# Kernel optimization log

Measured on AMD Instinct MI355X. Metric: run time of the kernel, lower is better.

Reference implementation:

```python
import jax, jax.numpy as jnp
import numpy as np

B, T, H = 128, 1024, 200
IN0, OUT = 8, 4  # GRU layer-0 input size (4 targets + 4 emotion), fc output dim


def setup_inputs() -> dict:
    key = jax.random.key(0)
    ks = jax.random.split(key, 12)
    s = 1.0 / np.sqrt(H)  # torch RNN default init: U(-1/sqrt(H), 1/sqrt(H))
    u = lambda k, shp: jax.random.uniform(k, shp, jnp.float32, -s, s)
    return {
        "x": jax.random.normal(ks[0], (B, T, IN0), jnp.float32),
        "W_ih0": u(ks[1], (3 * H, IN0)),
        "W_hh0": u(ks[2], (3 * H, H)),
        "b_ih0": u(ks[3], (3 * H,)),
        "b_hh0": u(ks[4], (3 * H,)),
        "W_ih1": u(ks[5], (3 * H, H)),
        "W_hh1": u(ks[6], (3 * H, H)),
        "b_ih1": u(ks[7], (3 * H,)),
        "b_hh1": u(ks[8], (3 * H,)),
        "W_fc": u(ks[9], (OUT, H)),
        "b_fc": u(ks[10], (OUT,)),
        "xlens": jax.random.randint(ks[11], (B,), 1, T + 1),
    }


def _gru_cell(h, gx, W_hh, b_hh):
    # torch GRU cell: gx = W_ih @ x + b_ih precomputed, gates order [r, z, n]
    gh = h @ W_hh.T + b_hh
    ir, iz, i_n = jnp.split(gx, 3, axis=-1)
    hr, hz, hn = jnp.split(gh, 3, axis=-1)
    r = jax.nn.sigmoid(ir + hr)
    z = jax.nn.sigmoid(iz + hz)
    n = jnp.tanh(i_n + r * hn)
    return (1.0 - z) * n + z * h


def _forward(x, W_ih0, W_hh0, b_ih0, b_hh0, W_ih1, W_hh1, b_ih1, b_hh1, W_fc, b_fc):
    b, t, _ = x.shape
    emotion = x[:, 0, -4:]                      # (B,4) frozen at t=0, as in source
    targets = x[:, :, :4]                       # (B,T,4)
    # step inputs: t=0 -> ones(B,4); t>0 -> targets[:, t-1] (teacher forcing)
    tf = jnp.concatenate([jnp.ones((b, 1, 4), x.dtype), targets[:, :-1, :]], axis=1)
    inputs = jnp.concatenate(
        [tf, jnp.broadcast_to(emotion[:, None, :], (b, t, 4))], axis=-1)  # (B,T,8)
    # precompute layer-0 input projections for all steps (one big GEMM)
    gx0 = jnp.einsum("btc,gc->btg", inputs, W_ih0) + b_ih0  # (B,T,3H)

    def step(carry, gx0_t):
        h0, h1 = carry
        h0 = _gru_cell(h0, gx0_t, W_hh0, b_hh0)
        gx1 = h0 @ W_ih1.T + b_ih1
        h1 = _gru_cell(h1, gx1, W_hh1, b_hh1)
        out = jnp.tanh(h1 @ W_fc.T + b_fc)      # fused fc + tanh
        return (h0, h1), out

    h0 = jnp.zeros((b, H), x.dtype)
    h1 = jnp.zeros((b, H), x.dtype)
    _, outs = jax.lax.scan(step, (h0, h1), jnp.swapaxes(gx0, 0, 1))  # (T,B,4)
    return jnp.swapaxes(outs, 0, 1)             # (B,T,4)


def reference(x, W_ih0, W_hh0, b_ih0, b_hh0, W_ih1, W_hh1, b_ih1, b_hh1, W_fc, b_fc, xlens):
    # xlens is accepted but unused, exactly as in the source forward()
    return _forward(x, W_ih0, W_hh0, b_ih0, b_hh0, W_ih1, W_hh1, b_ih1, b_hh1, W_fc, b_fc)
```

## Files before the change

kernel.cpp:

```cpp
#include <hip/hip_runtime.h>
#include <hip/hip_bf16.h>


#define TT 1024
#define HH 200
#define NB 16
#define HS 13
#define KP 232

typedef __attribute__((ext_vector_type(8))) short short8;
typedef __attribute__((ext_vector_type(4))) float f32x4;

__device__ __forceinline__ float sigm(float v) { return 1.0f / (1.0f + __expf(-v)); }
__device__ __forceinline__ float tanh_fast(float v) {
  float e = __expf(-2.0f * v);
  return (1.0f - e) / (1.0f + e);
}
__device__ __forceinline__ uint llc_load_u32(const uint* p) {
  return __hip_atomic_load(p, __ATOMIC_RELAXED, __HIP_MEMORY_SCOPE_SYSTEM);
}
__device__ __forceinline__ void llc_store_u32(uint* p, uint v) {
  __hip_atomic_store(p, v, __ATOMIC_RELAXED, __HIP_MEMORY_SCOPE_SYSTEM);
}
__device__ __forceinline__ float bfu2f(ushort u) {
  return __uint_as_float(((uint)u) << 16);
}
__device__ __forceinline__ ushort f2bfu(float f) {
  __hip_bfloat16 b = __float2bfloat16(f);
  return *(ushort*)&b;
}
__device__ __forceinline__ uint packf(float h) {
  ushort hi = f2bfu(h);
  float  fh = bfu2f(hi);
  ushort lo = f2bfu(h - fh);
  return (uint)hi | ((uint)lo << 16);
}

__global__ __launch_bounds__(256, 1) void gru2_mfma(
    const float* __restrict__ x,
    const float* __restrict__ Wih0, const float* __restrict__ Whh0,
    const float* __restrict__ bih0, const float* __restrict__ bhh0,
    const float* __restrict__ Wih1, const float* __restrict__ Whh1,
    const float* __restrict__ bih1, const float* __restrict__ bhh1,
    const float* __restrict__ Wfc,  const float* __restrict__ bfc,
    float* __restrict__ out,
    uint* __restrict__ h0g, uint* __restrict__ h1g, uint* __restrict__ syncp)
{
  __shared__ __align__(16) ushort hBh[2][NB][KP];
  __shared__ __align__(16) ushort hBl[2][NB][KP];
  __shared__ float D[117][17];
  __shared__ float Wi0t[8][39];
  __shared__ float bi0[39], bh0[39], bi1[39], bh1[39], bfs[4];
  __shared__ float xc[NB][8];

  const int tid  = threadIdx.x;
  const int wave = tid >> 6;
  const int lane = tid & 63;
  const int m15  = lane & 15;
  const int q    = lane >> 4;

  const int g  = blockIdx.x & 7;
  const int s  = blockIdx.x >> 3;
  const int b0 = g * NB;
  const int j0 = s * HS;
  const int hs = (HH - j0 < HS) ? (HH - j0) : HS;
  const int th   = 3 * hs;
  const int h0r  = 6 * hs;
  const int T0   = (h0r + 15) >> 4;
  const int NT   = T0 + ((th + 15) >> 4);
  const bool isOut = (s == 15);

  uint* flags = syncp;

  short8 Ah[2][7], Al[2][7];
  #pragma unroll
  for (int mt = 0; mt < 2; ++mt) {
    const int T = wave * 2 + mt;
    const bool fc  = isOut && (wave == 2) && (mt == 0);
    const bool val = fc || (T < NT);
    #pragma unroll
    for (int kt = 0; kt < 7; ++kt) {
      short8 vh = {0,0,0,0,0,0,0,0}, vl = {0,0,0,0,0,0,0,0};
      #pragma unroll
      for (int j = 0; j < 8; ++j) {
        const int k = kt * 32 + q * 8 + j;
        float w = 0.0f;
        if (val && k < HH) {
          if (fc) {
            if (m15 < 4) w = Wfc[m15 * HH + k];
          } else {
            const int p = T * 16 + m15;
            int r = -1;
            if (p < h0r) r = p;
            else if (p >= T0 * 16 && (p - T0 * 16) < th) r = h0r + (p - T0 * 16);
            if (r >= 0) {
              const int m  = r / th, rr = r - m * th;
              const int qq = rr / hs, jj = rr - qq * hs;
              const float* src = (m == 0) ? Whh0 : ((m == 1) ? Wih1 : Whh1);
              w = src[(qq * HH + j0 + jj) * HH + k];
            }
          }
        }
        const ushort uh = f2bfu(w);
        const ushort ul = f2bfu(w - bfu2f(uh));
        vh[j] = (short)uh; vl[j] = (short)ul;
      }
      Ah[mt][kt] = vh; Al[mt][kt] = vl;
    }
  }

  for (int u = tid; u < th * 8; u += 256) {
    int rr = u >> 3, c = u & 7;
    int qq = rr / hs, jj = rr - qq * hs;
    Wi0t[c][rr] = Wih0[(qq * HH + j0 + jj) * 8 + c];
  }
  for (int u = tid; u < th; u += 256) {
    int qq = u / hs, jj = u - qq * hs;
    int grow = qq * HH + j0 + jj;
    bi0[u] = bih0[grow]; bh0[u] = bhh0[grow];
    bi1[u] = bih1[grow]; bh1[u] = bhh1[grow];
  }
  if (tid < 4) bfs[tid] = bfc[tid];
  for (int u = tid; u < 2 * NB * KP / 2; u += 256) ((uint*)hBh)[u] = 0;
  for (int u = tid; u < 2 * NB * KP / 2; u += 256) ((uint*)hBl)[u] = 0;
  if (tid < 128 && (tid & 7) >= 4)
    xc[tid >> 3][tid & 7] = x[(b0 + (tid >> 3)) * TT * 8 + (tid & 7)];
  __syncthreads();

  const int gt = 16 * hs;
  const int cb = tid / hs;
  const int cj = tid - cb * hs;
  const int xb = tid >> 3, xcc7 = tid & 7;

  for (int t = 0; t <= TT + 1; ++t) {
    float xtf = 1.0f;
    if (tid < 128 && xcc7 < 4 && t > 0 && t < TT)
      xtf = x[((b0 + xb) * TT + (t - 1)) * 8 + xcc7];

    const uint* h0src = h0g + ((t + 1) & 1) * (128 * HH);
    const uint* h1src = h1g + (t & 1) * (128 * HH);
    uint tmp[25];
    #pragma unroll
    for (int i = 0; i < 25; ++i) {
      const int u  = tid + i * 256;
      const int st = u / 3200, rem = u - st * 3200;
      const int b  = rem / 200, k = rem - b * 200;
      tmp[i] = llc_load_u32(&(st ? h1src : h0src)[(b0 + b) * HH + k]);
    }
    #pragma unroll
    for (int i = 0; i < 25; ++i) {
      const int u  = tid + i * 256;
      const int st = u / 3200, rem = u - st * 3200;
      const int b  = rem / 200, k = rem - b * 200;
      hBh[st][b][k] = (ushort)(tmp[i] & 0xffff);
      hBl[st][b][k] = (ushort)(tmp[i] >> 16);
    }
    if (tid < 128 && xcc7 < 4 && t < TT)
      xc[xb][xcc7] = xtf;
    __syncthreads();

    #pragma unroll
    for (int mt = 0; mt < 2; ++mt) {
      const int T = wave * 2 + mt;
      const bool fc  = isOut && (wave == 2) && (mt == 0);
      const bool val = fc || (T < NT);
      if (!val) continue;
      const int st = fc ? 1 : ((T < T0) ? 0 : 1);
      const ushort* Bh = &hBh[st][m15][0];
      const ushort* Bl = &hBl[st][m15][0];
      f32x4 acc = {0.f, 0.f, 0.f, 0.f};
      #pragma unroll
      for (int kt = 0; kt < 7; ++kt) {
        const short8 bh = *(const short8*)&Bh[kt * 32 + q * 8];
        const short8 bl = *(const short8*)&Bl[kt * 32 + q * 8];
        acc = __builtin_amdgcn_mfma_f32_16x16x32_bf16(Ah[mt][kt], bh, acc, 0, 0, 0);
        acc = __builtin_amdgcn_mfma_f32_16x16x32_bf16(Ah[mt][kt], bl, acc, 0, 0, 0);
        acc = __builtin_amdgcn_mfma_f32_16x16x32_bf16(Al[mt][kt], bh, acc, 0, 0, 0);
      }
      if (fc) {
        if (t >= 2) {
          #pragma unroll
          for (int i = 0; i < 4; ++i) {
            const int p = q * 4 + i;
            if (p < 4)
              out[((b0 + m15) * TT + (t - 2)) * 4 + p] = tanh_fast(acc[i] + bfs[p]);
          }
        }
      } else {
        #pragma unroll
        for (int i = 0; i < 4; ++i) {
          const int p = T * 16 + q * 4 + i;
          int r = -1;
          if (p < h0r) r = p;
          else if (p >= T0 * 16 && (p - T0 * 16) < th) r = h0r + (p - T0 * 16);
          if (r >= 0) D[r][m15] = acc[i];
        }
      }
    }
    __syncthreads();

    if (tid < gt) {
      const float hv0 = bfu2f(hBh[0][cb][j0 + cj]) + bfu2f(hBl[0][cb][j0 + cj]);
      const float hv1 = bfu2f(hBh[1][cb][j0 + cj]) + bfu2f(hBl[1][cb][j0 + cj]);
      if (t < TT) {
        float ir = bi0[cj], iz = bi0[hs + cj], in_ = bi0[2 * hs + cj];
        #pragma unroll
        for (int c = 0; c < 8; ++c) {
          const float xv = xc[cb][c];
          ir  += Wi0t[c][cj] * xv;
          iz  += Wi0t[c][hs + cj] * xv;
          in_ += Wi0t[c][2 * hs + cj] * xv;
        }
        const float hr = D[cj][cb] + bh0[cj];
        const float hz = D[hs + cj][cb] + bh0[hs + cj];
        const float hn = D[2 * hs + cj][cb] + bh0[2 * hs + cj];
        const float r = sigm(ir + hr), z = sigm(iz + hz);
        const float n = tanh_fast(in_ + r * hn);
        llc_store_u32(&h0g[(t & 1) * (128 * HH) + (b0 + cb) * HH + j0 + cj],
                      packf((1.0f - z) * n + z * hv0));
      }
      if (t >= 1 && t <= TT) {
        const float ir  = D[3 * hs + cj][cb] + bi1[cj];
        const float iz  = D[4 * hs + cj][cb] + bi1[hs + cj];
        const float in_ = D[5 * hs + cj][cb] + bi1[2 * hs + cj];
        const float hr  = D[6 * hs + cj][cb] + bh1[cj];
        const float hz  = D[7 * hs + cj][cb] + bh1[hs + cj];
        const float hn  = D[8 * hs + cj][cb] + bh1[2 * hs + cj];
        const float r = sigm(ir + hr), z = sigm(iz + hz);
        const float n = tanh_fast(in_ + r * hn);
        llc_store_u32(&h1g[((t + 1) & 1) * (128 * HH) + (b0 + cb) * HH + j0 + cj],
                      packf((1.0f - z) * n + z * hv1));
      }
    }

    __syncthreads();
    if (tid == 0)
      llc_store_u32(&flags[g * 64 + s * 4], (uint)(t + 1));
    if (wave == 0) {
      const uint tgt = (uint)(t + 1);
      const uint* fp = &flags[g * 64 + (lane & 15) * 4];
      for (int it = 0; it < 200000; ++it) {
        uint v = tgt;
        if (lane < 16) v = llc_load_u32(fp);
        if (__all((int)(v >= tgt))) break;
        __builtin_amdgcn_s_sleep(1);
      }
    }
    __syncthreads();
  }
}

extern "C" void kernel_launch(void* const* d_in, const int* in_sizes, int n_in,
                              void* d_out, int out_size, void* d_ws, size_t ws_size,
                              hipStream_t stream) {
  uint* ws = (uint*)d_ws;
  hipMemsetAsync(d_ws, 0, (size_t)(102400 + 512) * sizeof(uint), stream);
  gru2_mfma<<<128, 256, 0, stream>>>(
      (const float*)d_in[0],
      (const float*)d_in[1], (const float*)d_in[2],
      (const float*)d_in[3], (const float*)d_in[4],
      (const float*)d_in[5], (const float*)d_in[6],
      (const float*)d_in[7], (const float*)d_in[8],
      (const float*)d_in[9], (const float*)d_in[10],
      (float*)d_out, ws, ws + 51200, ws + 102400);
}
```

Baseline: 2.926 ms.

## Interleave two 8-row batch groups per block to hide cross-block sync latency

Each block now processes two independent half-size batch groups (8 rows each) in alternation instead of one 16-row group. While one group's flag wait and global hidden-state loads are in flight, the block runs MFMA and gate work for the other group, overlapping the inter-block barrier with compute. The cost is MFMA tiles that are half zero padding, twice as many syncthreads per step, and more flag traffic. The spin timeout is also lowered.

```diff
diff --git a/kernel.cpp b/kernel.cpp
--- a/kernel.cpp
+++ b/kernel.cpp
@@ -4,7 +4,6 @@
 
 #define TT 1024
 #define HH 200
-#define NB 16
 #define HS 13
 #define KP 232
 
@@ -46,12 +45,13 @@
     float* __restrict__ out,
     uint* __restrict__ h0g, uint* __restrict__ h1g, uint* __restrict__ syncp)
 {
-  __shared__ __align__(16) ushort hBh[2][NB][KP];
-  __shared__ __align__(16) ushort hBl[2][NB][KP];
+  __shared__ __align__(16) ushort hBh[2][2][8][KP];
+  __shared__ __align__(16) ushort hBl[2][2][8][KP];
+  __shared__ __align__(16) ushort zrh[KP], zrl[KP];
   __shared__ float D[117][17];
   __shared__ float Wi0t[8][39];
   __shared__ float bi0[39], bh0[39], bi1[39], bh1[39], bfs[4];
-  __shared__ float xc[NB][8];
+  __shared__ float xc[2][8][8];
 
   const int tid  = threadIdx.x;
   const int wave = tid >> 6;
@@ -59,9 +59,10 @@
   const int m15  = lane & 15;
   const int q    = lane >> 4;
 
-  const int g  = blockIdx.x & 7;
-  const int s  = blockIdx.x >> 3;
-  const int b0 = g * NB;
+  const int blkg = blockIdx.x & 7;
+  const int s    = blockIdx.x >> 3;
+  const int gA   = blkg,      gB  = blkg + 8;
+  const int bbA  = gA * 8,    bbB = gB * 8;
   const int j0 = s * HS;
   const int hs = (HH - j0 < HS) ? (HH - j0) : HS;
   const int th   = 3 * hs;
@@ -121,44 +122,42 @@
     bi1[u] = bih1[grow]; bh1[u] = bhh1[grow];
   }
   if (tid < 4) bfs[tid] = bfc[tid];
-  for (int u = tid; u < 2 * NB * KP / 2; u += 256) ((uint*)hBh)[u] = 0;
-  for (int u = tid; u < 2 * NB * KP / 2; u += 256) ((uint*)hBl)[u] = 0;
-  if (tid < 128 && (tid & 7) >= 4)
-    xc[tid >> 3][tid & 7] = x[(b0 + (tid >> 3)) * TT * 8 + (tid & 7)];
+  for (int u = tid; u < 2 * 2 * 8 * KP / 2; u += 256) ((uint*)hBh)[u] = 0;
+  for (int u = tid; u < 2 * 2 * 8 * KP / 2; u += 256) ((uint*)hBl)[u] = 0;
+  for (int u = tid; u < KP / 2; u += 256) { ((uint*)zrh)[u] = 0; ((uint*)zrl)[u] = 0; }
+  if (tid < 64) {
+    const int gi = tid >> 5, rem = tid & 31, b = rem >> 2, c = 4 + (rem & 3);
+    const int bb = gi ? bbB : bbA;
+    xc[gi][b][c] = x[(bb + b) * TT * 8 + c];
+  }
   __syncthreads();
 
-  const int gt = 16 * hs;
-  const int cb = tid / hs;
-  const int cj = tid - cb * hs;
-  const int xb = tid >> 3, xcc7 = tid & 7;
-
-  for (int t = 0; t <= TT + 1; ++t) {
-    float xtf = 1.0f;
-    if (tid < 128 && xcc7 < 4 && t > 0 && t < TT)
-      xtf = x[((b0 + xb) * TT + (t - 1)) * 8 + xcc7];
-
-    const uint* h0src = h0g + ((t + 1) & 1) * (128 * HH);
-    const uint* h1src = h1g + (t & 1) * (128 * HH);
-    uint tmp[25];
+  auto issue_w = [&](uint* w, int bb, int tau) {
+    const uint* p0 = h0g + ((tau + 1) & 1) * 25600;
+    const uint* p1 = h1g + (tau & 1) * 25600;
     #pragma unroll
-    for (int i = 0; i < 25; ++i) {
-      const int u  = tid + i * 256;
-      const int st = u / 3200, rem = u - st * 3200;
-      const int b  = rem / 200, k = rem - b * 200;
-      tmp[i] = llc_load_u32(&(st ? h1src : h0src)[(b0 + b) * HH + k]);
-    }
+    for (int i = 0; i < 13; ++i) {
+      if (i < 12 || tid < 128) {
+        const int u = tid + i * 256;
+        const int st = u / 1600, rem = u - st * 1600;
+        const int b = rem / 200, k = rem - b * 200;
+        w[i] = llc_load_u32(&(st ? p1 : p0)[(bb + b) * HH + k]);
+      }
+    }
+  };
+  auto unpack_w = [&](const uint* w, int gi) {
     #pragma unroll
-    for (int i = 0; i < 25; ++i) {
-      const int u  = tid + i * 256;
-      const int st = u / 3200, rem = u - st * 3200;
-      const int b  = rem / 200, k = rem - b * 200;
-      hBh[st][b][k] = (ushort)(tmp[i] & 0xffff);
-      hBl[st][b][k] = (ushort)(tmp[i] >> 16);
-    }
-    if (tid < 128 && xcc7 < 4 && t < TT)
-      xc[xb][xcc7] = xtf;
-    __syncthreads();
-
+    for (int i = 0; i < 13; ++i) {
+      if (i < 12 || tid < 128) {
+        const int u = tid + i * 256;
+        const int st = u / 1600, rem = u - st * 1600;
+        const int b = rem / 200, k = rem - b * 200;
+        hBh[st][gi][b][k] = (ushort)(w[i] & 0xffff);
+        hBl[st][gi][b][k] = (ushort)(w[i] >> 16);
+      }
+    }
+  };
+  auto mfma_phase = [&](int gi, int bb, int t) {
     #pragma unroll
     for (int mt = 0; mt < 2; ++mt) {
       const int T = wave * 2 + mt;
@@ -166,8 +165,8 @@
       const bool val = fc || (T < NT);
       if (!val) continue;
       const int st = fc ? 1 : ((T < T0) ? 0 : 1);
-      const ushort* Bh = &hBh[st][m15][0];
-      const ushort* Bl = &hBl[st][m15][0];
+      const ushort* Bh = (m15 < 8) ? &hBh[st][gi][m15][0] : zrh;
+      const ushort* Bl = (m15 < 8) ? &hBl[st][gi][m15][0] : zrl;
       f32x4 acc = {0.f, 0.f, 0.f, 0.f};
       #pragma unroll
       for (int kt = 0; kt < 7; ++kt) {
@@ -178,12 +177,12 @@
         acc = __builtin_amdgcn_mfma_f32_16x16x32_bf16(Al[mt][kt], bh, acc, 0, 0, 0);
       }
       if (fc) {
-        if (t >= 2) {
+        if (t >= 2 && m15 < 8) {
           #pragma unroll
           for (int i = 0; i < 4; ++i) {
             const int p = q * 4 + i;
             if (p < 4)
-              out[((b0 + m15) * TT + (t - 2)) * 4 + p] = tanh_fast(acc[i] + bfs[p]);
+              out[((bb + m15) * TT + (t - 2)) * 4 + p] = tanh_fast(acc[i] + bfs[p]);
           }
         }
       } else {
@@ -197,56 +196,96 @@
         }
       }
     }
-    __syncthreads();
-
-    if (tid < gt) {
-      const float hv0 = bfu2f(hBh[0][cb][j0 + cj]) + bfu2f(hBl[0][cb][j0 + cj]);
-      const float hv1 = bfu2f(hBh[1][cb][j0 + cj]) + bfu2f(hBl[1][cb][j0 + cj]);
+  };
+  const int gcb = tid / hs, gcj = tid - gcb * hs;
+  auto gates_phase = [&](int gi, int bb, int t) {
+    if (tid < 8 * hs) {
+      const float hv0 = bfu2f(hBh[0][gi][gcb][j0 + gcj]) + bfu2f(hBl[0][gi][gcb][j0 + gcj]);
+      const float hv1 = bfu2f(hBh[1][gi][gcb][j0 + gcj]) + bfu2f(hBl[1][gi][gcb][j0 + gcj]);
       if (t < TT) {
-        float ir = bi0[cj], iz = bi0[hs + cj], in_ = bi0[2 * hs + cj];
+        float ir = bi0[gcj], iz = bi0[hs + gcj], in_ = bi0[2 * hs + gcj];
         #pragma unroll
         for (int c = 0; c < 8; ++c) {
-          const float xv = xc[cb][c];
-          ir  += Wi0t[c][cj] * xv;
-          iz  += Wi0t[c][hs + cj] * xv;
-          in_ += Wi0t[c][2 * hs + cj] * xv;
+          const float xv = xc[gi][gcb][c];
+          ir  += Wi0t[c][gcj] * xv;
+          iz  += Wi0t[c][hs + gcj] * xv;
+          in_ += Wi0t[c][2 * hs + gcj] * xv;
         }
-        const float hr = D[cj][cb] + bh0[cj];
-        const float hz = D[hs + cj][cb] + bh0[hs + cj];
-        const float hn = D[2 * hs + cj][cb] + bh0[2 * hs + cj];
+        const float hr = D[gcj][gcb] + bh0[gcj];
+        const float hz = D[hs + gcj][gcb] + bh0[hs + gcj];
+        const float hn = D[2 * hs + gcj][gcb] + bh0[2 * hs + gcj];
         const float r = sigm(ir + hr), z = sigm(iz + hz);
         const float n = tanh_fast(in_ + r * hn);
-        llc_store_u32(&h0g[(t & 1) * (128 * HH) + (b0 + cb) * HH + j0 + cj],
+        llc_store_u32(&h0g[(t & 1) * 25600 + (bb + gcb) * HH + j0 + gcj],
                       packf((1.0f - z) * n + z * hv0));
       }
       if (t >= 1 && t <= TT) {
-        const float ir  = D[3 * hs + cj][cb] + bi1[cj];
-        const float iz  = D[4 * hs + cj][cb] + bi1[hs + cj];
-        const float in_ = D[5 * hs + cj][cb] + bi1[2 * hs + cj];
-        const float hr  = D[6 * hs + cj][cb] + bh1[cj];
-        const float hz  = D[7 * hs + cj][cb] + bh1[hs + cj];
-        const float hn  = D[8 * hs + cj][cb] + bh1[2 * hs + cj];
+        const float ir  = D[3 * hs + gcj][gcb] + bi1[gcj];
+        const float iz  = D[4 * hs + gcj][gcb] + bi1[hs + gcj];
+        const float in_ = D[5 * hs + gcj][gcb] + bi1[2 * hs + gcj];
+        const float hr  = D[6 * hs + gcj][gcb] + bh1[gcj];
+        const float hz  = D[7 * hs + gcj][gcb] + bh1[hs + gcj];
+        const float hn  = D[8 * hs + gcj][gcb] + bh1[2 * hs + gcj];
         const float r = sigm(ir + hr), z = sigm(iz + hz);
         const float n = tanh_fast(in_ + r * hn);
-        llc_store_u32(&h1g[((t + 1) & 1) * (128 * HH) + (b0 + cb) * HH + j0 + cj],
+        llc_store_u32(&h1g[((t + 1) & 1) * 25600 + (bb + gcb) * HH + j0 + gcj],
                       packf((1.0f - z) * n + z * hv1));
       }
     }
-
-    __syncthreads();
-    if (tid == 0)
-      llc_store_u32(&flags[g * 64 + s * 4], (uint)(t + 1));
+  };
+  auto poll_check = [&](int gr, uint tgt, uint v) {
     if (wave == 0) {
-      const uint tgt = (uint)(t + 1);
-      const uint* fp = &flags[g * 64 + (lane & 15) * 4];
-      for (int it = 0; it < 200000; ++it) {
-        uint v = tgt;
+      const uint* fp = &flags[gr * 64 + (lane & 15) * 4];
+      for (int it = 0; it < 20000; ++it) {
+        if (__all((int)((lane < 16 ? v : tgt) >= tgt))) break;
+        __builtin_amdgcn_s_sleep(1);
         if (lane < 16) v = llc_load_u32(fp);
-        if (__all((int)(v >= tgt))) break;
-        __builtin_amdgcn_s_sleep(1);
-      }
-    }
-    __syncthreads();
+      }
+    }
+  };
+
+  uint wA[13], wB[13];
+  float xtfA = 1.0f, xtfB;
+  issue_w(wA, bbA, 0);
+
+  for (int t = 0; t <= TT + 1; ++t) {
+    unpack_w(wA, 0);
+    if (tid < 32 && t < TT) xc[0][tid >> 2][tid & 3] = xtfA;
+    __syncthreads();
+    uint vB = (uint)t;
+    if (wave == 0 && lane < 16)
+      vB = llc_load_u32(&flags[gB * 64 + (lane & 15) * 4]);
+    mfma_phase(0, bbA, t);
+    __syncthreads();
+    poll_check(gB, (uint)t, vB);
+    __syncthreads();
+    issue_w(wB, bbB, t);
+    xtfB = 1.0f;
+    if (tid < 32 && t > 0 && t < TT)
+      xtfB = x[((bbB + (tid >> 2)) * TT + (t - 1)) * 8 + (tid & 3)];
+    gates_phase(0, bbA, t);
+    __syncthreads();
+    if (tid == 0) llc_store_u32(&flags[gA * 64 + s * 4], (uint)(t + 1));
+
+    unpack_w(wB, 1);
+    if (tid < 32 && t < TT) xc[1][tid >> 2][tid & 3] = xtfB;
+    __syncthreads();
+    uint vA = (uint)(t + 1);
+    if (wave == 0 && lane < 16 && t < TT + 1)
+      vA = llc_load_u32(&flags[gA * 64 + (lane & 15) * 4]);
+    mfma_phase(1, bbB, t);
+    __syncthreads();
+    if (t < TT + 1) poll_check(gA, (uint)(t + 1), vA);
+    __syncthreads();
+    xtfA = 1.0f;
+    if (t < TT + 1) {
+      issue_w(wA, bbA, t + 1);
+      if (tid < 32 && t + 1 < TT)
+        xtfA = x[((bbA + (tid >> 2)) * TT + t) * 8 + (tid & 3)];
+    }
+    gates_phase(1, bbB, t);
+    __syncthreads();
+    if (tid == 0) llc_store_u32(&flags[gB * 64 + s * 4], (uint)(t + 1));
   }
 }
 
@@ -254,7 +293,7 @@
                               void* d_out, int out_size, void* d_ws, size_t ws_size,
                               hipStream_t stream) {
   uint* ws = (uint*)d_ws;
-  hipMemsetAsync(d_ws, 0, (size_t)(102400 + 512) * sizeof(uint), stream);
+  hipMemsetAsync(d_ws, 0, (size_t)(102400 + 1024) * sizeof(uint), stream);
   gru2_mfma<<<128, 256, 0, stream>>>(
       (const float*)d_in[0],
       (const float*)d_in[1], (const float*)d_in[2],
```

Result: slower. 4.985 ms (+70.4%).
